# Kernel tuning notes

Hardware: AMD Instinct MI355X
Metric: run time of the kernel (lower is better)

## Reference

```python
import jax, jax.numpy as jnp
import numpy as np

DIM = 2048
NUM_HEADS = 16
HEAD_DIM = DIM // NUM_HEADS  # 128
ROPE_BASE = 10000.0


def setup_inputs() -> dict:
    key = jax.random.key(0)
    k1, k2, k3 = jax.random.split(key, 3)
    B, S = 2, 2048
    x = jax.random.normal(k1, (B, S, DIM), dtype=jnp.float32)
    # causal mask: 1 where allowed (k <= q), 0 elsewhere
    mask = jnp.tril(jnp.ones((S, S), dtype=jnp.int32))
    # torch Linear(dim, 3*dim, bias=False): store transposed so y = x @ w
    w_qkv = jax.random.normal(k2, (DIM, 3 * DIM), dtype=jnp.float32) / np.sqrt(DIM)
    w_out = jax.random.normal(k3, (DIM, DIM), dtype=jnp.float32) / np.sqrt(DIM)
    return {"x": x, "w_qkv": w_qkv, "w_out": w_out, "mask": mask}


def _rope_cos_sin(seq_len, dtype):
    inv_freq = 1.0 / (ROPE_BASE ** (jnp.arange(0, HEAD_DIM, 2, dtype=jnp.float32) / HEAD_DIM))
    t = jnp.arange(seq_len, dtype=jnp.float32)
    freqs = t[:, None] * inv_freq[None, :]          # [S, D/2]
    emb = jnp.concatenate([freqs, freqs], axis=-1)  # [S, D]
    return jnp.cos(emb).astype(dtype), jnp.sin(emb).astype(dtype)


def _rotate_half(x):
    x1, x2 = jnp.split(x, 2, axis=-1)
    return jnp.concatenate([-x2, x1], axis=-1)


def reference(x, w_qkv, w_out, mask):
    B, S, _ = x.shape
    H, D = NUM_HEADS, HEAD_DIM
    qkv = x @ w_qkv                                   # [B, S, 3*dim]
    qkv = qkv.reshape(B, S, 3, H, D).transpose(2, 0, 3, 1, 4)  # [3, B, H, S, D]
    q, k, v = qkv[0], qkv[1], qkv[2]
    cos, sin = _rope_cos_sin(S, x.dtype)              # [S, D] broadcast over B,H
    q = q * cos + _rotate_half(q) * sin
    k = k * cos + _rotate_half(k) * sin
    scale = D ** -0.5
    score = jnp.einsum("bhqd,bhkd->bhqk", q, k) * scale
    score = jnp.where(mask == 0, -jnp.inf, score)
    attn = jax.nn.softmax(score, axis=-1)             # dropout = identity (eval)
    out = jnp.einsum("bhqk,bhkd->bhqd", attn, v)
    out = out.transpose(0, 2, 1, 3).reshape(B, S, H * D)
    return out @ w_out
```

## Files before the change

### kernel.cpp

```cpp
#include <hip/hip_runtime.h>

typedef __attribute__((ext_vector_type(8))) __bf16 bf16x8;
typedef __attribute__((ext_vector_type(4))) float f32x4;

__device__ __forceinline__ unsigned short f2bf(float x) {
  union { float f; unsigned int u; } v; v.f = x;
  unsigned int r = v.u + 0x7fffu + ((v.u >> 16) & 1u);
  return (unsigned short)(r >> 16);
}
__device__ __forceinline__ float bf2f(unsigned short x) {
  union { unsigned int u; float f; } v; v.u = ((unsigned int)x) << 16;
  return v.f;
}
__device__ __forceinline__ void g2l16(const void* g, void* l) {
  __builtin_amdgcn_global_load_lds((const __attribute__((address_space(1))) void*)g,
                                   (__attribute__((address_space(3))) void*)l, 16, 0, 0);
}

__global__ __launch_bounds__(256) void cvt_f32_bf16_k(const float* __restrict__ in,
                                                      unsigned short* __restrict__ out) {
  int i = blockIdx.x * 256 + threadIdx.x;
  float4 v = ((const float4*)in)[i];
  ushort4 o;
  o.x = f2bf(v.x); o.y = f2bf(v.y); o.z = f2bf(v.z); o.w = f2bf(v.w);
  ((ushort4*)out)[i] = o;
}

__global__ __launch_bounds__(256) void tr_cvt_k(const float* __restrict__ in,
                                                unsigned short* __restrict__ out,
                                                int R, int C) {
  __shared__ unsigned short t[64][65];
  int c0 = blockIdx.x * 64, r0 = blockIdx.y * 64;
  int tx = threadIdx.x & 63, tg = threadIdx.x >> 6;
#pragma unroll
  for (int i = 0; i < 16; i++) {
    int r = i * 4 + tg;
    t[r][tx] = f2bf(in[(size_t)(r0 + r) * C + c0 + tx]);
  }
  __syncthreads();
#pragma unroll
  for (int i = 0; i < 16; i++) {
    int c = i * 4 + tg;
    out[(size_t)(c0 + c) * R + r0 + tx] = t[tx][c];
  }
}

__global__ __launch_bounds__(256) void tr_b16_k(const unsigned short* __restrict__ in,
                                                unsigned short* __restrict__ out,
                                                int R, int C) {
  __shared__ unsigned short t[64][65];
  const size_t zoff = (size_t)blockIdx.z * R * C;
  int c0 = blockIdx.x * 64, r0 = blockIdx.y * 64;
  int tx = threadIdx.x & 63, tg = threadIdx.x >> 6;
#pragma unroll
  for (int i = 0; i < 16; i++) {
    int r = i * 4 + tg;
    t[r][tx] = in[zoff + (size_t)(r0 + r) * C + c0 + tx];
  }
  __syncthreads();
#pragma unroll
  for (int i = 0; i < 16; i++) {
    int c = i * 4 + tg;
    out[zoff + (size_t)(c0 + c) * R + r0 + tx] = t[tx][c];
  }
}

template <int EPI>
__global__ __launch_bounds__(256) void gemm_bt_k(const unsigned short* __restrict__ A,
                                                 const unsigned short* __restrict__ BT,
                                                 int K, int N,
                                                 float* __restrict__ outF,
                                                 unsigned short* __restrict__ oq,
                                                 unsigned short* __restrict__ ok,
                                                 unsigned short* __restrict__ ov) {
  __shared__ __align__(16) unsigned short lA[128 * 64];
  __shared__ __align__(16) unsigned short lB[128 * 64];
  const int tid = threadIdx.x;
  const int w = tid >> 6, lane = tid & 63;
  const int quad = lane >> 4, l16 = lane & 15;
  const int m0 = blockIdx.y * 128, n0 = blockIdx.x * 128;
  const int wm = (w >> 1) * 64, wn = (w & 1) * 64;
  f32x4 acc[4][4] = {};
  const int srow = tid >> 3;
  const int schunk = (tid & 7) ^ (srow & 7);
  const unsigned short* gA = A + (size_t)(m0 + srow) * K + schunk * 8;
  const unsigned short* gB = BT + (size_t)(n0 + srow) * K + schunk * 8;
  char* ldA = (char*)lA + tid * 16;
  char* ldB = (char*)lB + tid * 16;
  const size_t rskip = (size_t)32 * K;
  for (int k0 = 0; k0 < K; k0 += 64) {
#pragma unroll
    for (int j = 0; j < 4; j++) {
      g2l16(gA + k0 + j * rskip, ldA + j * 4096);
      g2l16(gB + k0 + j * rskip, ldB + j * 4096);
    }
    __syncthreads();
#pragma unroll
    for (int ks = 0; ks < 2; ks++) {
      bf16x8 af[4], bfv[4];
#pragma unroll
      for (int i = 0; i < 4; i++)
        af[i] = *(const bf16x8*)((const char*)lA + (size_t)(wm + i * 16 + l16) * 128 +
                                 ((size_t)((ks * 4 + quad) ^ (l16 & 7)) * 16));
#pragma unroll
      for (int j = 0; j < 4; j++)
        bfv[j] = *(const bf16x8*)((const char*)lB + (size_t)(wn + j * 16 + l16) * 128 +
                                  ((size_t)((ks * 4 + quad) ^ (l16 & 7)) * 16));
#pragma unroll
      for (int i = 0; i < 4; i++)
#pragma unroll
        for (int j = 0; j < 4; j++)
          acc[i][j] = __builtin_amdgcn_mfma_f32_16x16x32_bf16(af[i], bfv[j], acc[i][j], 0, 0, 0);
    }
    __syncthreads();
  }
  if (EPI == 0) {
    const int which = n0 >> 11;
    const int h = (n0 >> 7) & 15;
    unsigned short* dst = (which == 0) ? oq : (which == 1) ? ok : ov;
#pragma unroll
    for (int i = 0; i < 4; i++) {
#pragma unroll
      for (int r = 0; r < 4; r++) {
        int mm = m0 + wm + i * 16 + quad * 4 + r;
        int b = mm >> 11, s = mm & 2047;
        size_t rb = ((size_t)(b * 16 + h) * 2048 + s) * 128;
#pragma unroll
        for (int j = 0; j < 4; j++)
          dst[rb + wn + j * 16 + l16] = f2bf(acc[i][j][r]);
      }
    }
  } else {
#pragma unroll
    for (int i = 0; i < 4; i++)
#pragma unroll
      for (int r = 0; r < 4; r++) {
        size_t rowb = (size_t)(m0 + wm + i * 16 + quad * 4 + r) * N;
#pragma unroll
        for (int j = 0; j < 4; j++)
          outF[rowb + n0 + wn + j * 16 + l16] = acc[i][j][r];
      }
  }
}

__global__ __launch_bounds__(256) void rope_k(unsigned short* __restrict__ q,
                                              unsigned short* __restrict__ k) {
  const int bid = blockIdx.x;
  unsigned short* buf = (bid < 16384) ? q : k;
  const float scale = (bid < 16384) ? 0.08838834764831845f : 1.0f;
  int i = (bid & 16383) * 256 + threadIdx.x;
  int d = i & 63;
  int s = (i >> 6) & 2047;
  int bh = i >> 17;
  size_t base = ((size_t)bh * 2048 + s) * 128;
  float a = bf2f(buf[base + d]);
  float b = bf2f(buf[base + 64 + d]);
  float theta = (float)s * exp2f(-(float)d * (13.287712379549449f / 64.0f));
  float sn, cs;
  __sincosf(theta, &sn, &cs);
  buf[base + d] = f2bf((a * cs - b * sn) * scale);
  buf[base + 64 + d] = f2bf((b * cs + a * sn) * scale);
}

__global__ __launch_bounds__(256, 2) void attn_k(const unsigned short* __restrict__ qb,
                                                 const unsigned short* __restrict__ kb,
                                                 const unsigned short* __restrict__ vt,
                                                 unsigned short* __restrict__ ob) {
  __shared__ __align__(16) unsigned short lK[64 * 128];
  __shared__ __align__(16) unsigned short lV[128 * 64];
  __shared__ __align__(16) __bf16 pbuf[4][32 * 72];
  const int tid = threadIdx.x;
  const int w = tid >> 6, lane = tid & 63;
  const int quad = lane >> 4, l16 = lane & 15;
  const int qt = (blockIdx.y < 16) ? (int)blockIdx.x : 15 - (int)blockIdx.x;
  const int bh = blockIdx.y;
  const int bi = bh >> 4, h = bh & 15;
  const int q0w = qt * 128 + w * 32;
  const unsigned short* qp = qb + (size_t)bh * 2048 * 128;
  const unsigned short* kp = kb + (size_t)bh * 2048 * 128;
  const unsigned short* vp = vt + (size_t)bh * 128 * 2048;
  __bf16* pw = pbuf[w];

  bf16x8 qf[2][4];
#pragma unroll
  for (int rg = 0; rg < 2; rg++) {
    const unsigned short* qr = qp + (size_t)(q0w + rg * 16 + l16) * 128 + quad * 8;
#pragma unroll
    for (int st = 0; st < 4; st++) qf[rg][st] = *(const bf16x8*)(qr + st * 32);
  }
  f32x4 o[2][8] = {};
  f32x4 lsum[2] = {};

  const int krow = tid >> 4;
  const int kcg = (tid & 15) ^ krow;
  const int vd = tid >> 3;
  const int vsg = (tid & 7) ^ ((tid >> 3) & 7);
  unsigned short* lKdst = lK + (size_t)tid * 8;
  unsigned short* lVdst = lV + (size_t)tid * 8;

  const int nkt = 2 * qt + 2;
  const int myNkt = (q0w + 31) / 64 + 1;
  for (int kt = 0; kt < nkt; kt++) {
    const int kt0 = kt * 64;
#pragma unroll
    for (int j = 0; j < 4; j++) {
      g2l16(kp + (size_t)(kt0 + j * 16 + krow) * 128 + kcg * 8, lKdst + j * 2048);
      g2l16(vp + (size_t)(j * 32 + vd) * 2048 + kt0 + vsg * 8, lVdst + j * 2048);
    }
    __syncthreads();
    if (kt < myNkt) {
      f32x4 sc[2][4] = {};
#pragma unroll
      for (int ct = 0; ct < 4; ct++) {
        const int nrow = ct * 16 + l16;
#pragma unroll
        for (int st = 0; st < 4; st++) {
          bf16x8 kf = *(const bf16x8*)(lK + ((size_t)nrow * 16 + ((st * 4 + quad) ^ l16)) * 8);
          sc[0][ct] = __builtin_amdgcn_mfma_f32_16x16x32_bf16(qf[0][st], kf, sc[0][ct], 0, 0, 0);
          sc[1][ct] = __builtin_amdgcn_mfma_f32_16x16x32_bf16(qf[1][st], kf, sc[1][ct], 0, 0, 0);
        }
      }
      const bool needmask = (kt == myNkt - 1);
#pragma unroll
      for (int rg = 0; rg < 2; rg++)
#pragma unroll
        for (int ct = 0; ct < 4; ct++) {
          const int col = kt0 + ct * 16 + l16;
          const int rowb = q0w + rg * 16 + quad * 4;
#pragma unroll
          for (int r = 0; r < 4; r++) {
            float s = sc[rg][ct][r];
            if (needmask && col > rowb + r) s = -1e30f;
            float e = __expf(s);
            lsum[rg][r] += e;
            pw[(rg * 16 + quad * 4 + r) * 72 + ct * 16 + l16] = (__bf16)e;
          }
        }
      bf16x8 pf[2][2];
#pragma unroll
      for (int rg = 0; rg < 2; rg++)
#pragma unroll
        for (int sb = 0; sb < 2; sb++)
          pf[rg][sb] = *(const bf16x8*)(pw + (rg * 16 + l16) * 72 + sb * 32 + quad * 8);
#pragma unroll
      for (int dt = 0; dt < 8; dt++) {
#pragma unroll
        for (int sb = 0; sb < 2; sb++) {
          bf16x8 vf = *(const bf16x8*)(lV +
              ((size_t)(dt * 16 + l16) * 8 + ((sb * 4 + quad) ^ (l16 & 7))) * 8);
          o[0][dt] = __builtin_amdgcn_mfma_f32_16x16x32_bf16(pf[0][sb], vf, o[0][dt], 0, 0, 0);
          o[1][dt] = __builtin_amdgcn_mfma_f32_16x16x32_bf16(pf[1][sb], vf, o[1][dt], 0, 0, 0);
        }
      }
    }
    __syncthreads();
  }
#pragma unroll
  for (int m = 1; m < 16; m <<= 1)
#pragma unroll
    for (int rg = 0; rg < 2; rg++)
#pragma unroll
      for (int r = 0; r < 4; r++)
        lsum[rg][r] += __shfl_xor(lsum[rg][r], m, 64);
  float inv[2][4];
#pragma unroll
  for (int rg = 0; rg < 2; rg++)
#pragma unroll
    for (int r = 0; r < 4; r++) inv[rg][r] = 1.0f / lsum[rg][r];
#pragma unroll
  for (int rg = 0; rg < 2; rg++)
#pragma unroll
    for (int dt = 0; dt < 8; dt++)
#pragma unroll
      for (int r = 0; r < 4; r++)
        ob[(size_t)(bi * 2048 + q0w + rg * 16 + quad * 4 + r) * 2048 + h * 128 + dt * 16 + l16] =
            f2bf(o[rg][dt][r] * inv[rg][r]);
}

extern "C" void kernel_launch(void* const* d_in, const int* in_sizes, int n_in,
                              void* d_out, int out_size, void* d_ws, size_t ws_size,
                              hipStream_t stream) {
  const float* x = (const float*)d_in[0];
  const float* wqkv = (const float*)d_in[1];
  const float* wout = (const float*)d_in[2];
  char* ws = (char*)d_ws;
  const size_t MiB = 1ull << 20;
  unsigned short* xb    = (unsigned short*)(ws + 0);
  unsigned short* wqkvT = (unsigned short*)(ws + 16 * MiB);
  unsigned short* woutT = (unsigned short*)(ws + 40 * MiB);
  unsigned short* qb    = (unsigned short*)(ws + 48 * MiB);
  unsigned short* kb    = (unsigned short*)(ws + 64 * MiB);
  unsigned short* vb    = (unsigned short*)(ws + 80 * MiB);
  unsigned short* vtb   = (unsigned short*)(ws + 96 * MiB);
  unsigned short* attnb = (unsigned short*)(ws + 112 * MiB);
  float* outF = (float*)d_out;

  cvt_f32_bf16_k<<<8192, 256, 0, stream>>>(x, xb);
  tr_cvt_k<<<dim3(96, 32), 256, 0, stream>>>(wqkv, wqkvT, 2048, 6144);
  tr_cvt_k<<<dim3(32, 32), 256, 0, stream>>>(wout, woutT, 2048, 2048);
  gemm_bt_k<0><<<dim3(48, 32), 256, 0, stream>>>(xb, wqkvT, 2048, 6144, nullptr, qb, kb, vb);
  rope_k<<<32768, 256, 0, stream>>>(qb, kb);
  tr_b16_k<<<dim3(2, 32, 32), 256, 0, stream>>>(vb, vtb, 2048, 128);
  attn_k<<<dim3(16, 32), 256, 0, stream>>>(qb, kb, vtb, attnb);
  gemm_bt_k<1><<<dim3(16, 32), 256, 0, stream>>>(attnb, woutT, 2048, 2048, outF,
                                                 nullptr, nullptr, nullptr);
}
```

Baseline: 400.5 us.

## Fuse RoPE and V transpose into QKV GEMM epilogue, merge prep kernels, register-prefetch attention tiles

Merges the x conversion and both weight transposes into one prep kernel. Moves RoPE and the V transpose into the QKV GEMM epilogue through a padded LDS staging buffer, which removes two kernels and their round trips through global memory. The attention kernel now prefetches the next K/V tile into registers instead of loading it straight into LDS, so global loads can overlap with compute. The trade-off is higher register pressure and a heavier epilogue in attention and the GEMM.

```diff
diff --git a/kernel.cpp b/kernel.cpp
--- a/kernel.cpp
+++ b/kernel.cpp
@@ -17,21 +17,27 @@
                                    (__attribute__((address_space(3))) void*)l, 16, 0, 0);
 }
 
-__global__ __launch_bounds__(256) void cvt_f32_bf16_k(const float* __restrict__ in,
-                                                      unsigned short* __restrict__ out) {
-  int i = blockIdx.x * 256 + threadIdx.x;
-  float4 v = ((const float4*)in)[i];
-  ushort4 o;
-  o.x = f2bf(v.x); o.y = f2bf(v.y); o.z = f2bf(v.z); o.w = f2bf(v.w);
-  ((ushort4*)out)[i] = o;
-}
-
-__global__ __launch_bounds__(256) void tr_cvt_k(const float* __restrict__ in,
-                                                unsigned short* __restrict__ out,
-                                                int R, int C) {
+__global__ __launch_bounds__(256) void prep_k(const float* __restrict__ x,
+                                              const float* __restrict__ wq,
+                                              const float* __restrict__ wo,
+                                              unsigned short* __restrict__ xb,
+                                              unsigned short* __restrict__ wqT,
+                                              unsigned short* __restrict__ woT) {
   __shared__ unsigned short t[64][65];
-  int c0 = blockIdx.x * 64, r0 = blockIdx.y * 64;
-  int tx = threadIdx.x & 63, tg = threadIdx.x >> 6;
+  const int b = blockIdx.x;
+  if (b < 8192) {
+    int i = b * 256 + threadIdx.x;
+    float4 v = ((const float4*)x)[i];
+    ushort4 o;
+    o.x = f2bf(v.x); o.y = f2bf(v.y); o.z = f2bf(v.z); o.w = f2bf(v.w);
+    ((ushort4*)xb)[i] = o;
+    return;
+  }
+  const float* in; unsigned short* out; int C, c0, r0;
+  const int R = 2048;
+  if (b < 11264) { int bb = b - 8192;  in = wq; out = wqT; C = 6144; c0 = (bb % 96) * 64; r0 = (bb / 96) * 64; }
+  else           { int bb = b - 11264; in = wo; out = woT; C = 2048; c0 = (bb & 31) * 64; r0 = (bb >> 5) * 64; }
+  const int tx = threadIdx.x & 63, tg = threadIdx.x >> 6;
 #pragma unroll
   for (int i = 0; i < 16; i++) {
     int r = i * 4 + tg;
@@ -42,26 +48,6 @@
   for (int i = 0; i < 16; i++) {
     int c = i * 4 + tg;
     out[(size_t)(c0 + c) * R + r0 + tx] = t[tx][c];
-  }
-}
-
-__global__ __launch_bounds__(256) void tr_b16_k(const unsigned short* __restrict__ in,
-                                                unsigned short* __restrict__ out,
-                                                int R, int C) {
-  __shared__ unsigned short t[64][65];
-  const size_t zoff = (size_t)blockIdx.z * R * C;
-  int c0 = blockIdx.x * 64, r0 = blockIdx.y * 64;
-  int tx = threadIdx.x & 63, tg = threadIdx.x >> 6;
-#pragma unroll
-  for (int i = 0; i < 16; i++) {
-    int r = i * 4 + tg;
-    t[r][tx] = in[zoff + (size_t)(r0 + r) * C + c0 + tx];
-  }
-  __syncthreads();
-#pragma unroll
-  for (int i = 0; i < 16; i++) {
-    int c = i * 4 + tg;
-    out[zoff + (size_t)(c0 + c) * R + r0 + tx] = t[tx][c];
   }
 }
 
@@ -73,8 +59,9 @@
                                                  unsigned short* __restrict__ oq,
                                                  unsigned short* __restrict__ ok,
                                                  unsigned short* __restrict__ ov) {
-  __shared__ __align__(16) unsigned short lA[128 * 64];
-  __shared__ __align__(16) unsigned short lB[128 * 64];
+  __shared__ __align__(16) unsigned short smem[16640];
+  unsigned short* lA = smem;
+  unsigned short* lB = smem + 8192;
   const int tid = threadIdx.x;
   const int w = tid >> 6, lane = tid & 63;
   const int quad = lane >> 4, l16 = lane & 15;
@@ -117,17 +104,42 @@
   if (EPI == 0) {
     const int which = n0 >> 11;
     const int h = (n0 >> 7) & 15;
-    unsigned short* dst = (which == 0) ? oq : (which == 1) ? ok : ov;
-#pragma unroll
-    for (int i = 0; i < 4; i++) {
+#pragma unroll
+    for (int i = 0; i < 4; i++)
 #pragma unroll
       for (int r = 0; r < 4; r++) {
-        int mm = m0 + wm + i * 16 + quad * 4 + r;
-        int b = mm >> 11, s = mm & 2047;
-        size_t rb = ((size_t)(b * 16 + h) * 2048 + s) * 128;
+        int row = wm + i * 16 + quad * 4 + r;
 #pragma unroll
         for (int j = 0; j < 4; j++)
-          dst[rb + wn + j * 16 + l16] = f2bf(acc[i][j][r]);
+          smem[row * 130 + wn + j * 16 + l16] = f2bf(acc[i][j][r]);
+      }
+    __syncthreads();
+    const int bi2 = m0 >> 11, s0 = m0 & 2047;
+    if (which < 2) {
+      unsigned short* dst = (which == 0) ? oq : ok;
+      const float scale = (which == 0) ? 0.08838834764831845f : 1.0f;
+      const int d = tid & 63, tg = tid >> 6;
+      const float fr = exp2f(-(float)d * (13.287712379549449f / 64.0f));
+      const size_t hb = ((size_t)(bi2 * 16 + h) * 2048 + s0) * 128;
+#pragma unroll
+      for (int i = 0; i < 32; i++) {
+        int r = i * 4 + tg;
+        float a = bf2f(smem[r * 130 + d]);
+        float bb = bf2f(smem[r * 130 + 64 + d]);
+        float sn, cs;
+        __sincosf((float)(s0 + r) * fr, &sn, &cs);
+        dst[hb + (size_t)r * 128 + d]      = f2bf((a * cs - bb * sn) * scale);
+        dst[hb + (size_t)r * 128 + 64 + d] = f2bf((bb * cs + a * sn) * scale);
+      }
+    } else {
+      const int d = tid >> 1, sh = (tid & 1) * 64;
+      const size_t vr = ((size_t)(bi2 * 16 + h) * 128 + d) * 2048 + s0 + sh;
+#pragma unroll
+      for (int v = 0; v < 8; v++) {
+        unsigned short tmp[8];
+#pragma unroll
+        for (int e = 0; e < 8; e++) tmp[e] = smem[(sh + v * 8 + e) * 130 + d];
+        *(uint4*)(ov + vr + v * 8) = *(const uint4*)tmp;
       }
     }
   } else {
@@ -141,25 +153,6 @@
           outF[rowb + n0 + wn + j * 16 + l16] = acc[i][j][r];
       }
   }
-}
-
-__global__ __launch_bounds__(256) void rope_k(unsigned short* __restrict__ q,
-                                              unsigned short* __restrict__ k) {
-  const int bid = blockIdx.x;
-  unsigned short* buf = (bid < 16384) ? q : k;
-  const float scale = (bid < 16384) ? 0.08838834764831845f : 1.0f;
-  int i = (bid & 16383) * 256 + threadIdx.x;
-  int d = i & 63;
-  int s = (i >> 6) & 2047;
-  int bh = i >> 17;
-  size_t base = ((size_t)bh * 2048 + s) * 128;
-  float a = bf2f(buf[base + d]);
-  float b = bf2f(buf[base + 64 + d]);
-  float theta = (float)s * exp2f(-(float)d * (13.287712379549449f / 64.0f));
-  float sn, cs;
-  __sincosf(theta, &sn, &cs);
-  buf[base + d] = f2bf((a * cs - b * sn) * scale);
-  buf[base + 64 + d] = f2bf((b * cs + a * sn) * scale);
 }
 
 __global__ __launch_bounds__(256, 2) void attn_k(const unsigned short* __restrict__ qb,
@@ -200,14 +193,29 @@
 
   const int nkt = 2 * qt + 2;
   const int myNkt = (q0w + 31) / 64 + 1;
+
+  uint4 pk[4], pv[4];
+#pragma unroll
+  for (int j = 0; j < 4; j++) {
+    pk[j] = *(const uint4*)(kp + (size_t)(j * 16 + krow) * 128 + kcg * 8);
+    pv[j] = *(const uint4*)(vp + (size_t)(j * 32 + vd) * 2048 + vsg * 8);
+  }
   for (int kt = 0; kt < nkt; kt++) {
     const int kt0 = kt * 64;
 #pragma unroll
     for (int j = 0; j < 4; j++) {
-      g2l16(kp + (size_t)(kt0 + j * 16 + krow) * 128 + kcg * 8, lKdst + j * 2048);
-      g2l16(vp + (size_t)(j * 32 + vd) * 2048 + kt0 + vsg * 8, lVdst + j * 2048);
-    }
-    __syncthreads();
+      *(uint4*)(lKdst + j * 2048) = pk[j];
+      *(uint4*)(lVdst + j * 2048) = pv[j];
+    }
+    __syncthreads();
+    if (kt + 1 < nkt) {
+      const int kn = kt0 + 64;
+#pragma unroll
+      for (int j = 0; j < 4; j++) {
+        pk[j] = *(const uint4*)(kp + (size_t)(kn + j * 16 + krow) * 128 + kcg * 8);
+        pv[j] = *(const uint4*)(vp + (size_t)(j * 32 + vd) * 2048 + kn + vsg * 8);
+      }
+    }
     if (kt < myNkt) {
       f32x4 sc[2][4] = {};
 #pragma unroll
@@ -290,17 +298,12 @@
   unsigned short* woutT = (unsigned short*)(ws + 40 * MiB);
   unsigned short* qb    = (unsigned short*)(ws + 48 * MiB);
   unsigned short* kb    = (unsigned short*)(ws + 64 * MiB);
-  unsigned short* vb    = (unsigned short*)(ws + 80 * MiB);
-  unsigned short* vtb   = (unsigned short*)(ws + 96 * MiB);
-  unsigned short* attnb = (unsigned short*)(ws + 112 * MiB);
+  unsigned short* vtb   = (unsigned short*)(ws + 80 * MiB);
+  unsigned short* attnb = (unsigned short*)(ws + 96 * MiB);
   float* outF = (float*)d_out;
 
-  cvt_f32_bf16_k<<<8192, 256, 0, stream>>>(x, xb);
-  tr_cvt_k<<<dim3(96, 32), 256, 0, stream>>>(wqkv, wqkvT, 2048, 6144);
-  tr_cvt_k<<<dim3(32, 32), 256, 0, stream>>>(wout, woutT, 2048, 2048);
-  gemm_bt_k<0><<<dim3(48, 32), 256, 0, stream>>>(xb, wqkvT, 2048, 6144, nullptr, qb, kb, vb);
-  rope_k<<<32768, 256, 0, stream>>>(qb, kb);
-  tr_b16_k<<<dim3(2, 32, 32), 256, 0, stream>>>(vb, vtb, 2048, 128);
+  prep_k<<<12288, 256, 0, stream>>>(x, wqkv, wout, xb, wqkvT, woutT);
+  gemm_bt_k<0><<<dim3(48, 32), 256, 0, stream>>>(xb, wqkvT, 2048, 6144, nullptr, qb, kb, vtb);
   attn_k<<<dim3(16, 32), 256, 0, stream>>>(qb, kb, vtb, attnb);
   gemm_bt_k<1><<<dim3(16, 32), 256, 0, stream>>>(attnb, woutT, 2048, 2048, outF,
                                                  nullptr, nullptr, nullptr);
```

After: 438.5 us. 9.5% more time.
